# Optimization experiments

Hardware: AMD Instinct MI355X
Metric: run time of the kernel (lower is better)

Reference implementation:

```python
import jax, jax.numpy as jnp
import numpy as np

N_NODES = 100000
N_EDGES = 3200000
IN_F = 256
OUT_F = 256


def setup_inputs() -> dict:
    key = jax.random.key(0)
    k_x, k_r, k_c, k_v, k_w = jax.random.split(key, 5)
    x = jax.random.normal(k_x, (N_NODES, IN_F), dtype=jnp.float32)
    edge_rows = jax.random.randint(k_r, (N_EDGES,), 0, N_NODES, dtype=jnp.int32)
    edge_cols = jax.random.randint(k_c, (N_EDGES,), 0, N_NODES, dtype=jnp.int32)
    adj_vals = jax.random.uniform(k_v, (N_EDGES,), dtype=jnp.float32)
    # Xavier-uniform init as in nn.init.xavier_uniform_
    limit = float(np.sqrt(6.0 / (IN_F + OUT_F)))
    weight = jax.random.uniform(k_w, (IN_F, OUT_F), minval=-limit, maxval=limit, dtype=jnp.float32)
    bias = jnp.zeros((OUT_F,), dtype=jnp.float32)
    return {"x": x, "edge_rows": edge_rows, "edge_cols": edge_cols,
            "adj_vals": adj_vals, "weight": weight, "bias": bias}


def reference(x, edge_rows, edge_cols, adj_vals, weight, bias):
    # Dense feature transform + bias: h = x @ W + b  -> [N, OUT_F]
    h = x @ weight + bias
    # Sparse adjacency matmul (SpMM): out[r] = sum_e adj_vals[e] * h[edge_cols[e]]
    msgs = adj_vals[:, None] * h[edge_cols]  # [E, OUT_F]
    out = jax.ops.segment_sum(msgs, edge_rows, num_segments=N_NODES)
    return out
```

## Files before the change

### kernel.cpp

```cpp
#include <hip/hip_runtime.h>

#define N_NODES 100000
#define IN_F 256
#define OUT_F 256
#define NROWS N_NODES
#define NBLK ((NROWS + 255) / 256)
#define MSTRIPS (N_NODES / 32)
#define GEMM_BLOCKS ((MSTRIPS + 3) / 4)

typedef float f32x4 __attribute__((ext_vector_type(4)));
typedef __bf16 bf16x8 __attribute__((ext_vector_type(8)));

__global__ __launch_bounds__(256) void prep_w_kernel(const float* __restrict__ W,
                                                     __bf16* __restrict__ Wt) {
    int n = blockIdx.x;
    int k = threadIdx.x;
    Wt[n * IN_F + k] = (__bf16)W[k * OUT_F + n];
}

__global__ __launch_bounds__(256, 2) void gemm_count_kernel(const float* __restrict__ x,
                                                            const __bf16* __restrict__ Wt,
                                                            const float* __restrict__ bias,
                                                            __bf16* __restrict__ h,
                                                            const int* __restrict__ rows,
                                                            int* __restrict__ deg, int nE) {
    if (blockIdx.x >= GEMM_BLOCKS) {
        int i = (blockIdx.x - GEMM_BLOCKS) * 1024 + threadIdx.x * 4;
        if (i + 3 < nE) {
            int4 rr = *(const int4*)(rows + i);
            atomicAdd(&deg[rr.x], 1);
            atomicAdd(&deg[rr.y], 1);
            atomicAdd(&deg[rr.z], 1);
            atomicAdd(&deg[rr.w], 1);
        } else {
            for (int e = i; e < nE; ++e) atomicAdd(&deg[rows[e]], 1);
        }
        return;
    }

    int wave = (blockIdx.x << 2) | (threadIdx.x >> 6);
    if (wave >= MSTRIPS) return;
    int lane = threadIdx.x & 63;
    int r16 = lane & 15;
    int quad = lane >> 4;

    const float*  xp0 = x + (size_t)(wave * 32 + r16) * IN_F + quad * 8;
    const float*  xp1 = xp0 + (size_t)16 * IN_F;
    const __bf16* wp  = Wt + (size_t)r16 * IN_F + quad * 8;

    f32x4 acc[2][16];
#pragma unroll
    for (int m = 0; m < 2; ++m)
#pragma unroll
        for (int i = 0; i < 16; ++i) acc[m][i] = (f32x4){0.f, 0.f, 0.f, 0.f};

#pragma unroll
    for (int k0 = 0; k0 < IN_F; k0 += 32) {
        f32x4 x00 = *(const f32x4*)(xp0 + k0);
        f32x4 x01 = *(const f32x4*)(xp0 + k0 + 4);
        f32x4 x10 = *(const f32x4*)(xp1 + k0);
        f32x4 x11 = *(const f32x4*)(xp1 + k0 + 4);
        bf16x8 a0, a1;
#pragma unroll
        for (int j = 0; j < 4; ++j) {
            a0[j] = (__bf16)x00[j]; a0[j + 4] = (__bf16)x01[j];
            a1[j] = (__bf16)x10[j]; a1[j + 4] = (__bf16)x11[j];
        }
#pragma unroll
        for (int nt = 0; nt < 16; ++nt) {
            bf16x8 b = *(const bf16x8*)(wp + (size_t)nt * 16 * IN_F + k0);
            acc[0][nt] = __builtin_amdgcn_mfma_f32_16x16x32_bf16(a0, b, acc[0][nt], 0, 0, 0);
            acc[1][nt] = __builtin_amdgcn_mfma_f32_16x16x32_bf16(a1, b, acc[1][nt], 0, 0, 0);
        }
    }

#pragma unroll
    for (int m = 0; m < 2; ++m)
#pragma unroll
        for (int nt = 0; nt < 16; ++nt) {
            float bv = bias[nt * 16 + r16];
            __bf16* hp = h + (size_t)(wave * 32 + m * 16 + quad * 4) * OUT_F + nt * 16 + r16;
#pragma unroll
            for (int r = 0; r < 4; ++r)
                hp[(size_t)r * OUT_F] = (__bf16)(acc[m][nt][r] + bv);
        }
}

__global__ __launch_bounds__(256) void partial_kernel(const int* __restrict__ deg,
                                                      int* __restrict__ partial) {
    __shared__ int s[256];
    int i = blockIdx.x * 256 + threadIdx.x;
    s[threadIdx.x] = (i < NROWS) ? deg[i] : 0;
    __syncthreads();
    for (int d = 128; d > 0; d >>= 1) {
        if (threadIdx.x < d) s[threadIdx.x] += s[threadIdx.x + d];
        __syncthreads();
    }
    if (threadIdx.x == 0) partial[blockIdx.x] = s[0];
}

__global__ __launch_bounds__(512) void scan_partial_kernel(const int* __restrict__ partial,
                                                           int* __restrict__ blockoff,
                                                           int* __restrict__ row_start, int nE) {
    __shared__ int s[512];
    int t = threadIdx.x;
    int v = (t < NBLK) ? partial[t] : 0;
    s[t] = v;
    __syncthreads();
    for (int d = 1; d < 512; d <<= 1) {
        int u = (t >= d) ? s[t - d] : 0;
        __syncthreads();
        s[t] += u;
        __syncthreads();
    }
    if (t < NBLK) blockoff[t] = s[t] - v;
    if (t == 0) row_start[NROWS] = nE;
}

__global__ __launch_bounds__(256) void scan_rows_kernel(const int* __restrict__ deg,
                                                        const int* __restrict__ blockoff,
                                                        int* __restrict__ row_start) {
    __shared__ int s[256];
    int t = threadIdx.x;
    int i = blockIdx.x * 256 + t;
    int v = (i < NROWS) ? deg[i] : 0;
    s[t] = v;
    __syncthreads();
    for (int d = 1; d < 256; d <<= 1) {
        int u = (t >= d) ? s[t - d] : 0;
        __syncthreads();
        s[t] += u;
        __syncthreads();
    }
    if (i < NROWS) row_start[i] = blockoff[blockIdx.x] + s[t] - v;
}

__global__ __launch_bounds__(256) void scatter_kernel(const int* __restrict__ rows,
                                                      const int* __restrict__ cols,
                                                      const float* __restrict__ vals,
                                                      const int* __restrict__ row_start,
                                                      int* __restrict__ deg,
                                                      int2* __restrict__ sorted, int nE) {
    int e = blockIdx.x * 256 + threadIdx.x;
    if (e >= nE) return;
    int r = rows[e];
    int pos = row_start[r] + atomicSub(&deg[r], 1) - 1;
    sorted[pos] = make_int2(cols[e], __float_as_int(vals[e]));
}

__global__ __launch_bounds__(256) void spmm_csr_kernel(const int* __restrict__ row_start,
                                                       const long long* __restrict__ sorted,
                                                       const __bf16* __restrict__ h,
                                                       float* __restrict__ out) {
    int half = threadIdx.x >> 5;
    int sub  = threadIdx.x & 31;
    int r = blockIdx.x * 8 + half;
    int e0 = row_start[r];
    int e1 = row_start[r + 1];

    f32x4 a0 = {0.f,0.f,0.f,0.f}, a1 = {0.f,0.f,0.f,0.f};
    f32x4 b0 = {0.f,0.f,0.f,0.f}, b1 = {0.f,0.f,0.f,0.f};

    int e = e0;
    for (; e + 8 <= e1; e += 8) {
        long long p0 = __builtin_nontemporal_load(sorted + e + 0);
        long long p1 = __builtin_nontemporal_load(sorted + e + 1);
        long long p2 = __builtin_nontemporal_load(sorted + e + 2);
        long long p3 = __builtin_nontemporal_load(sorted + e + 3);
        long long p4 = __builtin_nontemporal_load(sorted + e + 4);
        long long p5 = __builtin_nontemporal_load(sorted + e + 5);
        long long p6 = __builtin_nontemporal_load(sorted + e + 6);
        long long p7 = __builtin_nontemporal_load(sorted + e + 7);
        bf16x8 g0 = ((const bf16x8*)(h + (size_t)(int)p0 * OUT_F))[sub];
        bf16x8 g1 = ((const bf16x8*)(h + (size_t)(int)p1 * OUT_F))[sub];
        bf16x8 g2 = ((const bf16x8*)(h + (size_t)(int)p2 * OUT_F))[sub];
        bf16x8 g3 = ((const bf16x8*)(h + (size_t)(int)p3 * OUT_F))[sub];
        bf16x8 g4 = ((const bf16x8*)(h + (size_t)(int)p4 * OUT_F))[sub];
        bf16x8 g5 = ((const bf16x8*)(h + (size_t)(int)p5 * OUT_F))[sub];
        bf16x8 g6 = ((const bf16x8*)(h + (size_t)(int)p6 * OUT_F))[sub];
        bf16x8 g7 = ((const bf16x8*)(h + (size_t)(int)p7 * OUT_F))[sub];
        float v0 = __int_as_float((int)(p0 >> 32));
        float v1 = __int_as_float((int)(p1 >> 32));
        float v2 = __int_as_float((int)(p2 >> 32));
        float v3 = __int_as_float((int)(p3 >> 32));
        float v4 = __int_as_float((int)(p4 >> 32));
        float v5 = __int_as_float((int)(p5 >> 32));
        float v6 = __int_as_float((int)(p6 >> 32));
        float v7 = __int_as_float((int)(p7 >> 32));
#pragma unroll
        for (int j = 0; j < 4; ++j) {
            a0[j] += v0 * (float)g0[j]; a1[j] += v0 * (float)g0[j + 4];
            b0[j] += v1 * (float)g1[j]; b1[j] += v1 * (float)g1[j + 4];
            a0[j] += v2 * (float)g2[j]; a1[j] += v2 * (float)g2[j + 4];
            b0[j] += v3 * (float)g3[j]; b1[j] += v3 * (float)g3[j + 4];
            a0[j] += v4 * (float)g4[j]; a1[j] += v4 * (float)g4[j + 4];
            b0[j] += v5 * (float)g5[j]; b1[j] += v5 * (float)g5[j + 4];
            a0[j] += v6 * (float)g6[j]; a1[j] += v6 * (float)g6[j + 4];
            b0[j] += v7 * (float)g7[j]; b1[j] += v7 * (float)g7[j + 4];
        }
    }
    for (; e < e1; ++e) {
        long long p = sorted[e];
        float v = __int_as_float((int)(p >> 32));
        bf16x8 g = ((const bf16x8*)(h + (size_t)(int)p * OUT_F))[sub];
#pragma unroll
        for (int j = 0; j < 4; ++j) {
            a0[j] += v * (float)g[j];
            a1[j] += v * (float)g[j + 4];
        }
    }
#pragma unroll
    for (int j = 0; j < 4; ++j) { a0[j] += b0[j]; a1[j] += b1[j]; }
    float* op = out + (size_t)r * OUT_F + sub * 8;
    ((f32x4*)op)[0] = a0;
    ((f32x4*)op)[1] = a1;
}

extern "C" void kernel_launch(void* const* d_in, const int* in_sizes, int n_in,
                              void* d_out, int out_size, void* d_ws, size_t ws_size,
                              hipStream_t stream) {
    const float* x         = (const float*)d_in[0];
    const int*   edge_rows = (const int*)d_in[1];
    const int*   edge_cols = (const int*)d_in[2];
    const float* adj_vals  = (const float*)d_in[3];
    const float* weight    = (const float*)d_in[4];
    const float* bias      = (const float*)d_in[5];
    float* out = (float*)d_out;
    int nE = in_sizes[1];

    char* w = (char*)d_ws;
    __bf16* h  = (__bf16*)w;  w += (size_t)N_NODES * OUT_F * sizeof(__bf16);
    __bf16* Wt = (__bf16*)w;  w += (size_t)IN_F * OUT_F * sizeof(__bf16);
    int* deg       = (int*)w; w += (size_t)NROWS * 4;
    int* row_start = (int*)w; w += (size_t)(NROWS + 1) * 4 + 12;
    int* partial   = (int*)w; w += (size_t)NBLK * 4;
    int* blockoff  = (int*)w; w += (size_t)NBLK * 4 + 8;
    int2* sorted   = (int2*)w;

    hipMemsetAsync(deg, 0, (size_t)NROWS * sizeof(int), stream);
    prep_w_kernel<<<OUT_F, IN_F, 0, stream>>>(weight, Wt);

    int countBlocks = (nE + 1023) / 1024;
    gemm_count_kernel<<<GEMM_BLOCKS + countBlocks, 256, 0, stream>>>(x, Wt, bias, h,
                                                                     edge_rows, deg, nE);

    partial_kernel<<<NBLK, 256, 0, stream>>>(deg, partial);
    scan_partial_kernel<<<1, 512, 0, stream>>>(partial, blockoff, row_start, nE);
    scan_rows_kernel<<<NBLK, 256, 0, stream>>>(deg, blockoff, row_start);
    int eBlocks = (nE + 255) / 256;
    scatter_kernel<<<eBlocks, 256, 0, stream>>>(edge_rows, edge_cols, adj_vals,
                                                row_start, deg, (int2*)sorted, nE);
    spmm_csr_kernel<<<NROWS / 8, 256, 0, stream>>>(row_start, (const long long*)sorted, h, out);
}
```

Before: 735.2 us.

## Prefetch CSR edges in SpMM, vectorize scatter with inclusive-scan cursors

The row scan now writes each row's inclusive end offset into deg, so the scatter can claim slots with a single atomicSub on that cursor and no longer reads row_start. The scatter handles four edges per thread using vector loads and nontemporal 64-bit stores. The SpMM kernel software-pipelines the loads of the next 8 packed edges while the current 8 h-row gathers are in flight, handles the tail as one padded 8-wide batch, and raises the launch-bounds occupancy hint. The added prefetch registers and occupancy target may pressure registers, and the padded tail loads redundant rows.

```diff
diff --git a/kernel.cpp b/kernel.cpp
--- a/kernel.cpp
+++ b/kernel.cpp
@@ -117,7 +117,7 @@
     if (t == 0) row_start[NROWS] = nE;
 }
 
-__global__ __launch_bounds__(256) void scan_rows_kernel(const int* __restrict__ deg,
+__global__ __launch_bounds__(256) void scan_rows_kernel(int* __restrict__ deg,
                                                         const int* __restrict__ blockoff,
                                                         int* __restrict__ row_start) {
     __shared__ int s[256];
@@ -132,26 +132,49 @@
         s[t] += u;
         __syncthreads();
     }
-    if (i < NROWS) row_start[i] = blockoff[blockIdx.x] + s[t] - v;
+    if (i < NROWS) {
+        int inc = blockoff[blockIdx.x] + s[t];
+        row_start[i] = inc - v;
+        deg[i] = inc;
+    }
 }
 
 __global__ __launch_bounds__(256) void scatter_kernel(const int* __restrict__ rows,
                                                       const int* __restrict__ cols,
                                                       const float* __restrict__ vals,
-                                                      const int* __restrict__ row_start,
-                                                      int* __restrict__ deg,
-                                                      int2* __restrict__ sorted, int nE) {
-    int e = blockIdx.x * 256 + threadIdx.x;
-    if (e >= nE) return;
-    int r = rows[e];
-    int pos = row_start[r] + atomicSub(&deg[r], 1) - 1;
-    sorted[pos] = make_int2(cols[e], __float_as_int(vals[e]));
-}
-
-__global__ __launch_bounds__(256) void spmm_csr_kernel(const int* __restrict__ row_start,
-                                                       const long long* __restrict__ sorted,
-                                                       const __bf16* __restrict__ h,
-                                                       float* __restrict__ out) {
+                                                      int* __restrict__ cursor,
+                                                      long long* __restrict__ sorted, int nE) {
+    int i = (blockIdx.x * 256 + threadIdx.x) * 4;
+    if (i + 3 < nE) {
+        int4 rr = *(const int4*)(rows + i);
+        int4 cc = *(const int4*)(cols + i);
+        float4 vv = *(const float4*)(vals + i);
+        int p0 = atomicSub(&cursor[rr.x], 1) - 1;
+        int p1 = atomicSub(&cursor[rr.y], 1) - 1;
+        int p2 = atomicSub(&cursor[rr.z], 1) - 1;
+        int p3 = atomicSub(&cursor[rr.w], 1) - 1;
+        long long e0 = (long long)(((unsigned long long)(unsigned)__float_as_int(vv.x) << 32) | (unsigned)cc.x);
+        long long e1 = (long long)(((unsigned long long)(unsigned)__float_as_int(vv.y) << 32) | (unsigned)cc.y);
+        long long e2 = (long long)(((unsigned long long)(unsigned)__float_as_int(vv.z) << 32) | (unsigned)cc.z);
+        long long e3 = (long long)(((unsigned long long)(unsigned)__float_as_int(vv.w) << 32) | (unsigned)cc.w);
+        __builtin_nontemporal_store(e0, sorted + p0);
+        __builtin_nontemporal_store(e1, sorted + p1);
+        __builtin_nontemporal_store(e2, sorted + p2);
+        __builtin_nontemporal_store(e3, sorted + p3);
+    } else {
+        for (int e = i; e < nE; ++e) {
+            int r = rows[e];
+            int pos = atomicSub(&cursor[r], 1) - 1;
+            long long pk = (long long)(((unsigned long long)(unsigned)__float_as_int(vals[e]) << 32) | (unsigned)cols[e]);
+            __builtin_nontemporal_store(pk, sorted + pos);
+        }
+    }
+}
+
+__global__ __launch_bounds__(256, 4) void spmm_csr_kernel(const int* __restrict__ row_start,
+                                                          const long long* __restrict__ sorted,
+                                                          const __bf16* __restrict__ h,
+                                                          float* __restrict__ out) {
     int half = threadIdx.x >> 5;
     int sub  = threadIdx.x & 31;
     int r = blockIdx.x * 8 + half;
@@ -162,55 +185,72 @@
     f32x4 b0 = {0.f,0.f,0.f,0.f}, b1 = {0.f,0.f,0.f,0.f};
 
     int e = e0;
-    for (; e + 8 <= e1; e += 8) {
-        long long p0 = __builtin_nontemporal_load(sorted + e + 0);
-        long long p1 = __builtin_nontemporal_load(sorted + e + 1);
-        long long p2 = __builtin_nontemporal_load(sorted + e + 2);
-        long long p3 = __builtin_nontemporal_load(sorted + e + 3);
-        long long p4 = __builtin_nontemporal_load(sorted + e + 4);
-        long long p5 = __builtin_nontemporal_load(sorted + e + 5);
-        long long p6 = __builtin_nontemporal_load(sorted + e + 6);
-        long long p7 = __builtin_nontemporal_load(sorted + e + 7);
-        bf16x8 g0 = ((const bf16x8*)(h + (size_t)(int)p0 * OUT_F))[sub];
-        bf16x8 g1 = ((const bf16x8*)(h + (size_t)(int)p1 * OUT_F))[sub];
-        bf16x8 g2 = ((const bf16x8*)(h + (size_t)(int)p2 * OUT_F))[sub];
-        bf16x8 g3 = ((const bf16x8*)(h + (size_t)(int)p3 * OUT_F))[sub];
-        bf16x8 g4 = ((const bf16x8*)(h + (size_t)(int)p4 * OUT_F))[sub];
-        bf16x8 g5 = ((const bf16x8*)(h + (size_t)(int)p5 * OUT_F))[sub];
-        bf16x8 g6 = ((const bf16x8*)(h + (size_t)(int)p6 * OUT_F))[sub];
-        bf16x8 g7 = ((const bf16x8*)(h + (size_t)(int)p7 * OUT_F))[sub];
-        float v0 = __int_as_float((int)(p0 >> 32));
-        float v1 = __int_as_float((int)(p1 >> 32));
-        float v2 = __int_as_float((int)(p2 >> 32));
-        float v3 = __int_as_float((int)(p3 >> 32));
-        float v4 = __int_as_float((int)(p4 >> 32));
-        float v5 = __int_as_float((int)(p5 >> 32));
-        float v6 = __int_as_float((int)(p6 >> 32));
-        float v7 = __int_as_float((int)(p7 >> 32));
-#pragma unroll
-        for (int j = 0; j < 4; ++j) {
-            a0[j] += v0 * (float)g0[j]; a1[j] += v0 * (float)g0[j + 4];
-            b0[j] += v1 * (float)g1[j]; b1[j] += v1 * (float)g1[j + 4];
-            a0[j] += v2 * (float)g2[j]; a1[j] += v2 * (float)g2[j + 4];
-            b0[j] += v3 * (float)g3[j]; b1[j] += v3 * (float)g3[j + 4];
-            a0[j] += v4 * (float)g4[j]; a1[j] += v4 * (float)g4[j + 4];
-            b0[j] += v5 * (float)g5[j]; b1[j] += v5 * (float)g5[j + 4];
-            a0[j] += v6 * (float)g6[j]; a1[j] += v6 * (float)g6[j + 4];
-            b0[j] += v7 * (float)g7[j]; b1[j] += v7 * (float)g7[j + 4];
-        }
-    }
-    for (; e < e1; ++e) {
-        long long p = sorted[e];
-        float v = __int_as_float((int)(p >> 32));
-        bf16x8 g = ((const bf16x8*)(h + (size_t)(int)p * OUT_F))[sub];
-#pragma unroll
-        for (int j = 0; j < 4; ++j) {
-            a0[j] += v * (float)g[j];
-            a1[j] += v * (float)g[j + 4];
-        }
-    }
-#pragma unroll
-    for (int j = 0; j < 4; ++j) { a0[j] += b0[j]; a1[j] += b1[j]; }
+    if (e + 8 <= e1) {
+        long long p[8];
+#pragma unroll
+        for (int j = 0; j < 8; ++j) p[j] = __builtin_nontemporal_load(sorted + e + j);
+        e += 8;
+        for (; e + 8 <= e1; e += 8) {
+            bf16x8 g[8];
+#pragma unroll
+            for (int j = 0; j < 8; ++j)
+                g[j] = ((const bf16x8*)(h + (size_t)(int)p[j] * OUT_F))[sub];
+            long long q[8];
+#pragma unroll
+            for (int j = 0; j < 8; ++j) q[j] = __builtin_nontemporal_load(sorted + e + j);
+#pragma unroll
+            for (int j = 0; j < 8; ++j) {
+                float v = __int_as_float((int)(p[j] >> 32));
+#pragma unroll
+                for (int k = 0; k < 4; ++k) {
+                    if (j & 1) { b0[k] += v * (float)g[j][k]; b1[k] += v * (float)g[j][k + 4]; }
+                    else       { a0[k] += v * (float)g[j][k]; a1[k] += v * (float)g[j][k + 4]; }
+                }
+            }
+#pragma unroll
+            for (int j = 0; j < 8; ++j) p[j] = q[j];
+        }
+        {
+            bf16x8 g[8];
+#pragma unroll
+            for (int j = 0; j < 8; ++j)
+                g[j] = ((const bf16x8*)(h + (size_t)(int)p[j] * OUT_F))[sub];
+#pragma unroll
+            for (int j = 0; j < 8; ++j) {
+                float v = __int_as_float((int)(p[j] >> 32));
+#pragma unroll
+                for (int k = 0; k < 4; ++k) {
+                    if (j & 1) { b0[k] += v * (float)g[j][k]; b1[k] += v * (float)g[j][k + 4]; }
+                    else       { a0[k] += v * (float)g[j][k]; a1[k] += v * (float)g[j][k + 4]; }
+                }
+            }
+        }
+    }
+    if (e < e1) {
+        int rem = e1 - e;
+        long long t[8];
+#pragma unroll
+        for (int j = 0; j < 8; ++j) {
+            int idx = e + j;
+            if (idx > e1 - 1) idx = e1 - 1;
+            t[j] = __builtin_nontemporal_load(sorted + idx);
+        }
+        bf16x8 g[8];
+#pragma unroll
+        for (int j = 0; j < 8; ++j)
+            g[j] = ((const bf16x8*)(h + (size_t)(int)t[j] * OUT_F))[sub];
+#pragma unroll
+        for (int j = 0; j < 8; ++j) {
+            float v = (j < rem) ? __int_as_float((int)(t[j] >> 32)) : 0.f;
+#pragma unroll
+            for (int k = 0; k < 4; ++k) {
+                if (j & 1) { b0[k] += v * (float)g[j][k]; b1[k] += v * (float)g[j][k + 4]; }
+                else       { a0[k] += v * (float)g[j][k]; a1[k] += v * (float)g[j][k + 4]; }
+            }
+        }
+    }
+#pragma unroll
+    for (int k = 0; k < 4; ++k) { a0[k] += b0[k]; a1[k] += b1[k]; }
     float* op = out + (size_t)r * OUT_F + sub * 8;
     ((f32x4*)op)[0] = a0;
     ((f32x4*)op)[1] = a1;
@@ -235,7 +275,7 @@
     int* row_start = (int*)w; w += (size_t)(NROWS + 1) * 4 + 12;
     int* partial   = (int*)w; w += (size_t)NBLK * 4;
     int* blockoff  = (int*)w; w += (size_t)NBLK * 4 + 8;
-    int2* sorted   = (int2*)w;
+    long long* sorted = (long long*)w;
 
     hipMemsetAsync(deg, 0, (size_t)NROWS * sizeof(int), stream);
     prep_w_kernel<<<OUT_F, IN_F, 0, stream>>>(weight, Wt);
@@ -247,8 +287,8 @@
     partial_kernel<<<NBLK, 256, 0, stream>>>(deg, partial);
     scan_partial_kernel<<<1, 512, 0, stream>>>(partial, blockoff, row_start, nE);
     scan_rows_kernel<<<NBLK, 256, 0, stream>>>(deg, blockoff, row_start);
-    int eBlocks = (nE + 255) / 256;
-    scatter_kernel<<<eBlocks, 256, 0, stream>>>(edge_rows, edge_cols, adj_vals,
-                                                row_start, deg, (int2*)sorted, nE);
-    spmm_csr_kernel<<<NROWS / 8, 256, 0, stream>>>(row_start, (const long long*)sorted, h, out);
-}
+    int scatterBlocks = (nE + 1023) / 1024;
+    scatter_kernel<<<scatterBlocks, 256, 0, stream>>>(edge_rows, edge_cols, adj_vals,
+                                                      deg, sorted, nE);
+    spmm_csr_kernel<<<NROWS / 8, 256, 0, stream>>>(row_start, sorted, h, out);
+}
```

Measured after the change: 845.4 us. +15.0%, slower.
